# Performance work log

Hardware: AMD Instinct MI355X
Metric: run time of the kernel (lower is better)

The kernel has to match this reference:

```python
import jax, jax.numpy as jnp
import numpy as np
import math

B, L, H, E = 4, 2048, 16, 64

def setup_inputs() -> dict:
    key = jax.random.key(0)
    kq, kk, kv = jax.random.split(key, 3)
    queries = jax.random.normal(kq, (B, L, H, E), dtype=jnp.float32)
    keys = jax.random.normal(kk, (B, L, H, E), dtype=jnp.float32)
    values = jax.random.normal(kv, (B, L, H, E), dtype=jnp.float32)
    return {"queries": queries, "keys": keys, "values": values}

def reference(queries, keys, values):
    # queries: [B,L,H,E], keys: [B,S,H,E], values: [B,S,H,D]
    Bq, Lq, Hq, Eq = queries.shape
    scale = 1.0 / math.sqrt(Eq)
    scores = jnp.einsum('blhe,bshe->bhls', queries, keys)  # [B,H,L,S]
    Sq = keys.shape[1]
    causal = jnp.triu(jnp.ones((Lq, Sq), dtype=bool), k=1)  # True above diagonal
    scores = jnp.where(causal[None, None], -jnp.inf, scores)
    A = jax.nn.softmax(scale * scores, axis=-1)  # dropout is identity in eval
    V = jnp.einsum('bhls,bshd->blhd', A, values)
    return V
```

## Files before the change

### kernel.cpp

```cpp
#include <hip/hip_runtime.h>
#include <hip/hip_bf16.h>

typedef __attribute__((ext_vector_type(8))) short bf16x8;
typedef __attribute__((ext_vector_type(4))) short bf16x4;
typedef __attribute__((ext_vector_type(4))) float f32x4;
typedef __attribute__((ext_vector_type(16))) float f32x16;

#define NB 4
#define NL 2048
#define NH 16
#define NE 64
#define HE (NH*NE)
#define QW 32
#define QBLK 128
#define NQT (NL/QBLK)
#define NPAIR (NQT/2)
#define NBH 64
#define NKT 32
#define TILE_IMG 16384
#define WS_NEED ((size_t)NBH * NKT * TILE_IMG)
#define QSCALE (0.125f * 1.44269504088896340736f)

__device__ __forceinline__ unsigned pk2(float a, float b) {
  float2 t; t.x = a; t.y = b;
  __hip_bfloat162 hh = __float22bfloat162_rn(t);
  union { __hip_bfloat162 h; unsigned u; } v; v.h = hh;
  return v.u;
}
__device__ __forceinline__ void pswap(unsigned &a, unsigned &b) {
  auto r = __builtin_amdgcn_permlane32_swap(a, b, false, false);
  a = r[0]; b = r[1];
}
#define SWZ(row,col) ((row)*128 + ((col) ^ ((((row) ^ ((row)>>2)) & 7) << 4)))

__device__ __forceinline__ void cp16(unsigned char* lds, const unsigned char* g) {
  __builtin_amdgcn_global_load_lds(
      (const __attribute__((address_space(1))) unsigned int*)g,
      (__attribute__((address_space(3))) unsigned int*)lds, 16, 0, 0);
}

__global__ __launch_bounds__(256) void fa_stage(
    const float* __restrict__ K, const float* __restrict__ V,
    unsigned char* __restrict__ img)
{
  const int tid = threadIdx.x;
  const int bid = blockIdx.x;
  const int bh  = bid >> 5;
  const int t0  = bid & 31;
  const int h = bh & (NH-1), b = bh >> 4;
  const size_t base = ((size_t)b * NL * NH + h) * NE + (size_t)(t0 * 64) * HE;
  unsigned char* kimg = img + (size_t)(bh * NKT + t0) * TILE_IMG;
  unsigned char* vimg = kimg + 8192;
  #pragma unroll
  for (int rep = 0; rep < 2; ++rep) {
    const int idx = rep * 256 + tid;
    const int row = idx >> 3, gr = idx & 7;
    const float* kp = K + base + (size_t)row * HE + gr * 8;
    f32x4 a0 = *(const f32x4*)kp;
    f32x4 a1 = *(const f32x4*)(kp + 4);
    union { unsigned u[4]; bf16x8 v; } w;
    w.u[0] = pk2(a0[0], a0[1]); w.u[1] = pk2(a0[2], a0[3]);
    w.u[2] = pk2(a1[0], a1[1]); w.u[3] = pk2(a1[2], a1[3]);
    *(bf16x8*)(kimg + SWZ(row, gr * 16)) = w.v;
  }
  const int trow = tid >> 4, tcol = (tid & 15) * 4, sq = trow * 4;
  f32x4 vr[4];
  #pragma unroll
  for (int i = 0; i < 4; ++i)
    vr[i] = *(const f32x4*)(V + base + (size_t)(sq + i) * HE + tcol);
  #pragma unroll
  for (int j = 0; j < 4; ++j) {
    const int er = tcol + j;
    union { unsigned u[2]; bf16x4 v; } w;
    w.u[0] = pk2(vr[0][j], vr[1][j]);
    w.u[1] = pk2(vr[2][j], vr[3][j]);
    *(bf16x4*)(vimg + SWZ(er, sq * 2)) = w.v;
  }
}

#define PACK(SC, PA0, PA1)                                                     \
      l_run += (((SC[0]+SC[1])+(SC[2]+SC[3]))+((SC[4]+SC[5])+(SC[6]+SC[7])))   \
             + (((SC[8]+SC[9])+(SC[10]+SC[11]))+((SC[12]+SC[13])+(SC[14]+SC[15])));\
      {                                                                        \
        unsigned c0 = pk2(SC[0],SC[1]),   c1 = pk2(SC[2],SC[3]);               \
        unsigned c2 = pk2(SC[4],SC[5]),   c3 = pk2(SC[6],SC[7]);               \
        unsigned c4 = pk2(SC[8],SC[9]),   c5 = pk2(SC[10],SC[11]);             \
        unsigned c6 = pk2(SC[12],SC[13]), c7 = pk2(SC[14],SC[15]);             \
        pswap(c0, c2);  pswap(c1, c3);                                         \
        pswap(c4, c6);  pswap(c5, c7);                                         \
        PA0.u[0]=c0; PA0.u[1]=c1; PA0.u[2]=c2; PA0.u[3]=c3;                    \
        PA1.u[0]=c4; PA1.u[1]=c5; PA1.u[2]=c6; PA1.u[3]=c7;                    \
      }

#define SMPACK(SC, PA0, PA1)                                                   \
      _Pragma("unroll")                                                        \
      for (int r = 0; r < 16; ++r) SC[r] = exp2f(SC[r]);                       \
      PACK(SC, PA0, PA1)

#define STEP(IT, BUF)                                                          \
    {                                                                          \
      if ((IT) + 1 < nt) { asm volatile("s_waitcnt vmcnt(4)" ::: "memory"); }  \
      else               { asm volatile("s_waitcnt vmcnt(0)" ::: "memory"); }  \
      __builtin_amdgcn_sched_barrier(0);                                       \
      __builtin_amdgcn_s_barrier();                                            \
      __builtin_amdgcn_sched_barrier(0);                                       \
      if ((IT) + 2 < nt) {                                                     \
        unsigned char* kd = &k_lds[((BUF)+2)&3][0];                            \
        unsigned char* vd = &v_lds[((BUF)+2)&3][0];                            \
        cp16(kd + wb,        src_pf);                                          \
        cp16(kd + 4096 + wb, src_pf + 4096);                                   \
        cp16(vd + wb,        src_pf + 8192);                                   \
        cp16(vd + 4096 + wb, src_pf + 12288);                                  \
        src_pf += TILE_IMG;                                                    \
      }                                                                        \
      const int kv0 = (IT)*64;                                                 \
      if (kv0 + 63 <= qb) {                                                    \
        f32x16 sc0 = (f32x16)0.0f, sc1 = (f32x16)0.0f;                         \
        _Pragma("unroll")                                                      \
        for (int ks = 0; ks < 4; ++ks) {                                       \
          bf16x8 af0 = *(const bf16x8*)(&k_lds[BUF][0] + addr4[ks]);           \
          bf16x8 af1 = *(const bf16x8*)(&k_lds[BUF][0] + addr4[ks] + 4096);    \
          sc0 = __builtin_amdgcn_mfma_f32_32x32x16_bf16(af0, qf[ks], sc0,0,0,0);\
          sc1 = __builtin_amdgcn_mfma_f32_32x32x16_bf16(af1, qf[ks], sc1,0,0,0);\
        }                                                                      \
        union { unsigned u[4]; bf16x8 v; } a00, a01, a10, a11;                 \
        SMPACK(sc0, a00, a01)                                                  \
        SMPACK(sc1, a10, a11)                                                  \
        _Pragma("unroll")                                                      \
        for (int dt = 0; dt < 2; ++dt) {                                       \
          bf16x8 v00 = *(const bf16x8*)(&v_lds[BUF][0] + addr4[0] + dt*4096);  \
          bf16x8 v01 = *(const bf16x8*)(&v_lds[BUF][0] + addr4[1] + dt*4096);  \
          bf16x8 v10 = *(const bf16x8*)(&v_lds[BUF][0] + addr4[2] + dt*4096);  \
          bf16x8 v11 = *(const bf16x8*)(&v_lds[BUF][0] + addr4[3] + dt*4096);  \
          oacc2[0][dt] = __builtin_amdgcn_mfma_f32_32x32x16_bf16(              \
              v00, a00.v, oacc2[0][dt], 0, 0, 0);                              \
          oacc2[1][dt] = __builtin_amdgcn_mfma_f32_32x32x16_bf16(              \
              v10, a10.v, oacc2[1][dt], 0, 0, 0);                              \
          oacc2[0][dt] = __builtin_amdgcn_mfma_f32_32x32x16_bf16(              \
              v01, a01.v, oacc2[0][dt], 0, 0, 0);                              \
          oacc2[1][dt] = __builtin_amdgcn_mfma_f32_32x32x16_bf16(              \
              v11, a11.v, oacc2[1][dt], 0, 0, 0);                              \
        }                                                                      \
      } else {                                                                 \
        _Pragma("unroll")                                                      \
        for (int sub = 0; sub < 2; ++sub) {                                    \
          const int kv0s = kv0 + sub*32;                                       \
          if (kv0s <= qb + QW - 1) {                                           \
            f32x16 sc = (f32x16)0.0f;                                          \
            _Pragma("unroll")                                                  \
            for (int ks = 0; ks < 4; ++ks) {                                   \
              bf16x8 af = *(const bf16x8*)(&k_lds[BUF][0] + addr4[ks] + sub*4096);\
              sc = __builtin_amdgcn_mfma_f32_32x32x16_bf16(af, qf[ks], sc,0,0,0);\
            }                                                                  \
            _Pragma("unroll")                                                  \
            for (int r = 0; r < 16; ++r) {                                     \
              const int kvg = kv0s + (r&3) + 8*(r>>2) + 4*hi;                  \
              sc[r] = (kvg > qg) ? 0.0f : exp2f(sc[r]);                        \
            }                                                                  \
            union { unsigned u[4]; bf16x8 v; } pa0, pa1;                       \
            PACK(sc, pa0, pa1)                                                 \
            _Pragma("unroll")                                                  \
            for (int dt = 0; dt < 2; ++dt) {                                   \
              _Pragma("unroll")                                                \
              for (int ks2 = 0; ks2 < 2; ++ks2) {                              \
                bf16x8 av = *(const bf16x8*)(&v_lds[BUF][0] +                  \
                    addr4[sub*2 + ks2] + dt*4096);                             \
                oacc2[sub][dt] = __builtin_amdgcn_mfma_f32_32x32x16_bf16(      \
                    av, ks2 ? pa1.v : pa0.v, oacc2[sub][dt], 0, 0, 0);         \
              }                                                                \
            }                                                                  \
          }                                                                    \
        }                                                                      \
      }                                                                        \
    }

#define QTILE_SETUP()                                                          \
    bf16x8 qf[4];                                                              \
    {                                                                          \
      const float* qp = Qb + (size_t)(qb + ln) * HE + hi * 8;                  \
      _Pragma("unroll")                                                        \
      for (int ks = 0; ks < 4; ++ks) {                                         \
        f32x4 a0 = *(const f32x4*)(qp + ks*16);                                \
        f32x4 a1 = *(const f32x4*)(qp + ks*16 + 4);                            \
        union { unsigned u[4]; bf16x8 v; } f;                                  \
        f.u[0] = pk2(a0[0]*QSCALE, a0[1]*QSCALE);                              \
        f.u[1] = pk2(a0[2]*QSCALE, a0[3]*QSCALE);                              \
        f.u[2] = pk2(a1[0]*QSCALE, a1[1]*QSCALE);                              \
        f.u[3] = pk2(a1[2]*QSCALE, a1[3]*QSCALE);                              \
        qf[ks] = f.v;                                                          \
      }                                                                        \
    }                                                                          \
    f32x16 oacc2[2][2];                                                        \
    oacc2[0][0] = (f32x16)0.0f; oacc2[0][1] = (f32x16)0.0f;                    \
    oacc2[1][0] = (f32x16)0.0f; oacc2[1][1] = (f32x16)0.0f;                    \
    float l_run = 0.0f;

__global__ __launch_bounds__(256, 2) void fa_fwd(
    const float* __restrict__ Q, const unsigned char* __restrict__ img,
    float* __restrict__ O)
{
  __shared__ unsigned char k_lds[4][8192];
  __shared__ unsigned char v_lds[4][8192];

  const int tid  = threadIdx.x;
  const int lane = tid & 63;
  const int wid  = tid >> 6;
  const int hi   = lane >> 5;
  const int ln   = lane & 31;

  const int bidp = blockIdx.x;
  const int lb   = (bidp & 7) * 64 + (bidp >> 3);
  const int pair = lb & 7;
  const int bh   = lb >> 3;
  const int h    = bh & (NH-1);
  const int b    = bh >> 4;

  const size_t base = ((size_t)b * NL * NH + h) * NE;
  const float* Qb = Q + base;
  float*       Ob = O + base;
  const unsigned char* bimg = img + (size_t)bh * NKT * TILE_IMG;

  int addr4[4];
  {
    const int F = ((ln ^ (ln >> 2)) & 7) << 4;
    #pragma unroll
    for (int j = 0; j < 4; ++j) addr4[j] = ln*128 + ((j*32 + hi*16) ^ F);
  }
  const int wb = wid << 10;

  #pragma unroll 1
  for (int hf = 0; hf < 2; ++hf) {
    const int qt = hf ? (NQT - 1 - pair) : pair;
    const int q0 = qt * QBLK;
    const int qb = q0 + wid * QW;
    const int nt = qt * 2 + 2;
    const int qg = qb + ln;

    QTILE_SETUP()

    asm volatile("s_waitcnt vmcnt(0)" ::: "memory");
    __builtin_amdgcn_sched_barrier(0);
    __builtin_amdgcn_s_barrier();
    const unsigned char* src_pf = bimg + (size_t)tid * 16;
    cp16(&k_lds[0][0] + wb,        src_pf);
    cp16(&k_lds[0][0] + 4096 + wb, src_pf + 4096);
    cp16(&v_lds[0][0] + wb,        src_pf + 8192);
    cp16(&v_lds[0][0] + 4096 + wb, src_pf + 12288);
    src_pf += TILE_IMG;
    cp16(&k_lds[1][0] + wb,        src_pf);
    cp16(&k_lds[1][0] + 4096 + wb, src_pf + 4096);
    cp16(&v_lds[1][0] + wb,        src_pf + 8192);
    cp16(&v_lds[1][0] + 4096 + wb, src_pf + 12288);
    src_pf += TILE_IMG;

    int bs = 0;
    #pragma unroll 1
    for (; bs + 4 <= nt; bs += 4) {
      STEP(bs + 0, 0)
      STEP(bs + 1, 1)
      STEP(bs + 2, 2)
      STEP(bs + 3, 3)
    }
    if (bs < nt) {
      STEP(bs + 0, 0)
      STEP(bs + 1, 1)
    }

    const float l_tot = l_run + __shfl_xor(l_run, 32);
    const float inv = 1.0f / l_tot;
    float* op = Ob + (size_t)(qb + ln) * HE;
    #pragma unroll
    for (int dt = 0; dt < 2; ++dt)
      #pragma unroll
      for (int rq = 0; rq < 4; ++rq) {
        f32x4 w;
        w[0]=(oacc2[0][dt][rq*4+0]+oacc2[1][dt][rq*4+0])*inv;
        w[1]=(oacc2[0][dt][rq*4+1]+oacc2[1][dt][rq*4+1])*inv;
        w[2]=(oacc2[0][dt][rq*4+2]+oacc2[1][dt][rq*4+2])*inv;
        w[3]=(oacc2[0][dt][rq*4+3]+oacc2[1][dt][rq*4+3])*inv;
        *(f32x4*)(op + dt*32 + 8*rq + 4*hi) = w;
      }
  }
}

__global__ __launch_bounds__(256, 3) void fa_fwd_fused(
    const float* __restrict__ Q, const float* __restrict__ K,
    const float* __restrict__ V, float* __restrict__ O)
{
  __shared__ unsigned char kf_lds[2][64*128];
  __shared__ unsigned char vf_lds[2][64*128];
  const int tid  = threadIdx.x;
  const int lane = tid & 63;
  const int wid  = tid >> 6;
  const int hi   = lane >> 5;
  const int ln   = lane & 31;
  const int trow = tid >> 4;
  const int tcol = (tid & 15) * 4;
  const int sq   = trow * 4;
  const int bidp = blockIdx.x;
  const int lb   = (bidp & 7) * 64 + (bidp >> 3);
  const int pair = lb & 7;
  const int bh   = lb >> 3;
  const int h    = bh & (NH-1);
  const int b    = bh >> 4;
  const size_t base = ((size_t)b * NL * NH + h) * NE;
  const float* Qb = Q + base;
  const float* Kb = K + base;
  const float* Vb = V + base;
  float*       Ob = O + base;
  int cur = 0;
  #pragma unroll 1
  for (int hf = 0; hf < 2; ++hf) {
    const int qt = hf ? (NQT - 1 - pair) : pair;
    const int q0 = qt * QBLK;
    const int qb = q0 + wid * QW;
    const int nt = qt * 2 + 2;
    const int qg = qb + ln;
    bf16x8 qf[4];
    {
      const float* qp = Qb + (size_t)(qb + ln) * HE + hi * 8;
      #pragma unroll
      for (int ks = 0; ks < 4; ++ks) {
        f32x4 a0 = *(const f32x4*)(qp + ks*16);
        f32x4 a1 = *(const f32x4*)(qp + ks*16 + 4);
        union { unsigned u[4]; bf16x8 v; } f;
        f.u[0] = pk2(a0[0]*QSCALE, a0[1]*QSCALE);
        f.u[1] = pk2(a0[2]*QSCALE, a0[3]*QSCALE);
        f.u[2] = pk2(a1[0]*QSCALE, a1[1]*QSCALE);
        f.u[3] = pk2(a1[2]*QSCALE, a1[3]*QSCALE);
        qf[ks] = f.v;
      }
    }
    f32x16 oacc[2];
    oacc[0] = (f32x16)0.0f; oacc[1] = (f32x16)0.0f;
    float l_run = 0.0f;
    f32x4 kreg[4], vreg[4];
    #pragma unroll
    for (int p = 0; p < 4; ++p)
      kreg[p] = *(const f32x4*)(Kb + (size_t)(trow + p*16) * HE + tcol);
    #pragma unroll
    for (int i = 0; i < 4; ++i)
      vreg[i] = *(const f32x4*)(Vb + (size_t)(sq + i) * HE + tcol);
    #pragma unroll 1
    for (int it = 0; it < nt; ++it) {
      unsigned char* kb = kf_lds[cur];
      unsigned char* vb = vf_lds[cur];
      #pragma unroll
      for (int p = 0; p < 4; ++p) {
        const int row = trow + p*16;
        union { unsigned u[2]; bf16x4 v; } w;
        w.u[0] = pk2(kreg[p][0], kreg[p][1]);
        w.u[1] = pk2(kreg[p][2], kreg[p][3]);
        *(bf16x4*)(kb + SWZ(row, tcol*2)) = w.v;
      }
      #pragma unroll
      for (int j = 0; j < 4; ++j) {
        const int er = tcol + j;
        union { unsigned u[2]; bf16x4 v; } w;
        w.u[0] = pk2(vreg[0][j], vreg[1][j]);
        w.u[1] = pk2(vreg[2][j], vreg[3][j]);
        *(bf16x4*)(vb + SWZ(er, sq*2)) = w.v;
      }
      if (it + 1 < nt) {
        const int s0 = (it + 1) * 64;
        #pragma unroll
        for (int p = 0; p < 4; ++p)
          kreg[p] = *(const f32x4*)(Kb + (size_t)(s0 + trow + p*16) * HE + tcol);
        #pragma unroll
        for (int i = 0; i < 4; ++i)
          vreg[i] = *(const f32x4*)(Vb + (size_t)(s0 + sq + i) * HE + tcol);
      }
      asm volatile("s_waitcnt lgkmcnt(0)" ::: "memory");
      __builtin_amdgcn_sched_barrier(0);
      __builtin_amdgcn_s_barrier();
      __builtin_amdgcn_sched_barrier(0);
      #pragma unroll
      for (int sub = 0; sub < 2; ++sub) {
        const int kv0s = it*64 + sub*32;
        if (kv0s <= qb + QW - 1) {
          f32x16 sc = (f32x16)0.0f;
          #pragma unroll
          for (int ks = 0; ks < 4; ++ks) {
            const int kvr = sub*32 + ln;
            bf16x8 af = *(const bf16x8*)(kb + SWZ(kvr, ks*32 + hi*16));
            sc = __builtin_amdgcn_mfma_f32_32x32x16_bf16(af, qf[ks], sc, 0, 0, 0);
          }
          if (kv0s + 31 > qb) {
            #pragma unroll
            for (int r = 0; r < 16; ++r) {
              const int kvg = kv0s + (r&3) + 8*(r>>2) + 4*hi;
              sc[r] = (kvg > qg) ? 0.0f : exp2f(sc[r]);
            }
          } else {
            #pragma unroll
            for (int r = 0; r < 16; ++r) sc[r] = exp2f(sc[r]);
          }
          float s0_ = (sc[0]+sc[1])+(sc[2]+sc[3]);
          float s1_ = (sc[4]+sc[5])+(sc[6]+sc[7]);
          float s2_ = (sc[8]+sc[9])+(sc[10]+sc[11]);
          float s3_ = (sc[12]+sc[13])+(sc[14]+sc[15]);
          l_run += (s0_+s1_)+(s2_+s3_);
          unsigned c0 = pk2(sc[0],sc[1]),   c1 = pk2(sc[2],sc[3]);
          unsigned c2 = pk2(sc[4],sc[5]),   c3 = pk2(sc[6],sc[7]);
          unsigned c4 = pk2(sc[8],sc[9]),   c5 = pk2(sc[10],sc[11]);
          unsigned c6 = pk2(sc[12],sc[13]), c7 = pk2(sc[14],sc[15]);
          pswap(c0, c2);  pswap(c1, c3);
          pswap(c4, c6);  pswap(c5, c7);
          union { unsigned u[4]; bf16x8 v; } pa0, pa1;
          pa0.u[0]=c0; pa0.u[1]=c1; pa0.u[2]=c2; pa0.u[3]=c3;
          pa1.u[0]=c4; pa1.u[1]=c5; pa1.u[2]=c6; pa1.u[3]=c7;
          #pragma unroll
          for (int dt = 0; dt < 2; ++dt) {
            const int dr = dt*32 + ln;
            #pragma unroll
            for (int ks2 = 0; ks2 < 2; ++ks2) {
              bf16x8 av = *(const bf16x8*)(vb + SWZ(dr, sub*64 + ks2*32 + hi*16));
              oacc[dt] = __builtin_amdgcn_mfma_f32_32x32x16_bf16(
                  av, ks2 ? pa1.v : pa0.v, oacc[dt], 0, 0, 0);
            }
          }
        }
      }
      cur ^= 1;
    }
    const float l_tot = l_run + __shfl_xor(l_run, 32);
    const float inv = 1.0f / l_tot;
    float* op = Ob + (size_t)(qb + ln) * HE;
    #pragma unroll
    for (int dt = 0; dt < 2; ++dt)
      #pragma unroll
      for (int rq = 0; rq < 4; ++rq) {
        f32x4 w;
        w[0]=oacc[dt][rq*4+0]*inv; w[1]=oacc[dt][rq*4+1]*inv;
        w[2]=oacc[dt][rq*4+2]*inv; w[3]=oacc[dt][rq*4+3]*inv;
        *(f32x4*)(op + dt*32 + 8*rq + 4*hi) = w;
      }
  }
}

extern "C" void kernel_launch(void* const* d_in, const int* in_sizes, int n_in,
                              void* d_out, int out_size, void* d_ws, size_t ws_size,
                              hipStream_t stream) {
  const float* Q = (const float*)d_in[0];
  const float* K = (const float*)d_in[1];
  const float* V = (const float*)d_in[2];
  float* O = (float*)d_out;
  if (ws_size >= WS_NEED) {
    fa_stage<<<dim3(NBH * NKT), dim3(256), 0, stream>>>(K, V, (unsigned char*)d_ws);
    fa_fwd<<<dim3(NB * NH * NPAIR), dim3(256), 0, stream>>>(
        Q, (const unsigned char*)d_ws, O);
  } else {
    fa_fwd_fused<<<dim3(NB * NH * NPAIR), dim3(256), 0, stream>>>(Q, K, V, O);
  }
}
```

Before: 85.85 us.

## Software-pipeline PV matmul one tile behind QK and compute row sums via MFMA

Restructures the main attention loop so the P·V MFMAs for the previous KV tile run after the current tile's QK^T and exp, keeping the packed probabilities in registers across steps. This lets the exp and pack work overlap with the matrix unit. The scalar row-sum reduction is replaced by MFMAs against an all-ones bf16 fragment, which moves VALU adds onto the matrix core. The denominator is now summed from bf16-rounded probabilities, which slightly changes numerics, and the extra live fragments raise register pressure. The fallback path also changes to a per-step shuffle reduction.

```diff
diff --git a/kernel.cpp b/kernel.cpp
--- a/kernel.cpp
+++ b/kernel.cpp
@@ -20,6 +20,8 @@
 #define TILE_IMG 16384
 #define WS_NEED ((size_t)NBH * NKT * TILE_IMG)
 #define QSCALE (0.125f * 1.44269504088896340736f)
+
+union Pfrag { unsigned u[4]; bf16x8 v; };
 
 __device__ __forceinline__ unsigned pk2(float a, float b) {
   float2 t; t.x = a; t.y = b;
@@ -58,7 +60,7 @@
     const float* kp = K + base + (size_t)row * HE + gr * 8;
     f32x4 a0 = *(const f32x4*)kp;
     f32x4 a1 = *(const f32x4*)(kp + 4);
-    union { unsigned u[4]; bf16x8 v; } w;
+    Pfrag w;
     w.u[0] = pk2(a0[0], a0[1]); w.u[1] = pk2(a0[2], a0[3]);
     w.u[2] = pk2(a1[0], a1[1]); w.u[3] = pk2(a1[2], a1[3]);
     *(bf16x8*)(kimg + SWZ(row, gr * 16)) = w.v;
@@ -79,8 +81,6 @@
 }
 
 #define PACK(SC, PA0, PA1)                                                     \
-      l_run += (((SC[0]+SC[1])+(SC[2]+SC[3]))+((SC[4]+SC[5])+(SC[6]+SC[7])))   \
-             + (((SC[8]+SC[9])+(SC[10]+SC[11]))+((SC[12]+SC[13])+(SC[14]+SC[15])));\
       {                                                                        \
         unsigned c0 = pk2(SC[0],SC[1]),   c1 = pk2(SC[2],SC[3]);               \
         unsigned c2 = pk2(SC[4],SC[5]),   c3 = pk2(SC[6],SC[7]);               \
@@ -90,12 +90,33 @@
         pswap(c4, c6);  pswap(c5, c7);                                         \
         PA0.u[0]=c0; PA0.u[1]=c1; PA0.u[2]=c2; PA0.u[3]=c3;                    \
         PA1.u[0]=c4; PA1.u[1]=c5; PA1.u[2]=c6; PA1.u[3]=c7;                    \
-      }
+      }                                                                        \
+      l_acc = __builtin_amdgcn_mfma_f32_32x32x16_bf16(ones.v, PA0.v, l_acc,0,0,0);\
+      l_acc = __builtin_amdgcn_mfma_f32_32x32x16_bf16(ones.v, PA1.v, l_acc,0,0,0);
 
 #define SMPACK(SC, PA0, PA1)                                                   \
       _Pragma("unroll")                                                        \
       for (int r = 0; r < 16; ++r) SC[r] = exp2f(SC[r]);                       \
       PACK(SC, PA0, PA1)
+
+#define PVSTEP(VBUF)                                                           \
+    {                                                                          \
+      _Pragma("unroll")                                                        \
+      for (int dt = 0; dt < 2; ++dt) {                                         \
+        bf16x8 v00 = *(const bf16x8*)(&v_lds[VBUF][0] + addr4[0] + dt*4096);   \
+        bf16x8 v01 = *(const bf16x8*)(&v_lds[VBUF][0] + addr4[1] + dt*4096);   \
+        bf16x8 v10 = *(const bf16x8*)(&v_lds[VBUF][0] + addr4[2] + dt*4096);   \
+        bf16x8 v11 = *(const bf16x8*)(&v_lds[VBUF][0] + addr4[3] + dt*4096);   \
+        oacc2[0][dt] = __builtin_amdgcn_mfma_f32_32x32x16_bf16(                \
+            v00, p00.v, oacc2[0][dt], 0, 0, 0);                                \
+        oacc2[1][dt] = __builtin_amdgcn_mfma_f32_32x32x16_bf16(                \
+            v10, p10.v, oacc2[1][dt], 0, 0, 0);                                \
+        oacc2[0][dt] = __builtin_amdgcn_mfma_f32_32x32x16_bf16(                \
+            v01, p01.v, oacc2[0][dt], 0, 0, 0);                                \
+        oacc2[1][dt] = __builtin_amdgcn_mfma_f32_32x32x16_bf16(                \
+            v11, p11.v, oacc2[1][dt], 0, 0, 0);                                \
+      }                                                                        \
+    }
 
 #define STEP(IT, BUF)                                                          \
     {                                                                          \
@@ -113,6 +134,7 @@
         cp16(vd + 4096 + wb, src_pf + 12288);                                  \
         src_pf += TILE_IMG;                                                    \
       }                                                                        \
+      Pfrag n00, n01, n10, n11;                                                \
       const int kv0 = (IT)*64;                                                 \
       if (kv0 + 63 <= qb) {                                                    \
         f32x16 sc0 = (f32x16)0.0f, sc1 = (f32x16)0.0f;                         \
@@ -123,55 +145,46 @@
           sc0 = __builtin_amdgcn_mfma_f32_32x32x16_bf16(af0, qf[ks], sc0,0,0,0);\
           sc1 = __builtin_amdgcn_mfma_f32_32x32x16_bf16(af1, qf[ks], sc1,0,0,0);\
         }                                                                      \
-        union { unsigned u[4]; bf16x8 v; } a00, a01, a10, a11;                 \
-        SMPACK(sc0, a00, a01)                                                  \
-        SMPACK(sc1, a10, a11)                                                  \
-        _Pragma("unroll")                                                      \
-        for (int dt = 0; dt < 2; ++dt) {                                       \
-          bf16x8 v00 = *(const bf16x8*)(&v_lds[BUF][0] + addr4[0] + dt*4096);  \
-          bf16x8 v01 = *(const bf16x8*)(&v_lds[BUF][0] + addr4[1] + dt*4096);  \
-          bf16x8 v10 = *(const bf16x8*)(&v_lds[BUF][0] + addr4[2] + dt*4096);  \
-          bf16x8 v11 = *(const bf16x8*)(&v_lds[BUF][0] + addr4[3] + dt*4096);  \
-          oacc2[0][dt] = __builtin_amdgcn_mfma_f32_32x32x16_bf16(              \
-              v00, a00.v, oacc2[0][dt], 0, 0, 0);                              \
-          oacc2[1][dt] = __builtin_amdgcn_mfma_f32_32x32x16_bf16(              \
-              v10, a10.v, oacc2[1][dt], 0, 0, 0);                              \
-          oacc2[0][dt] = __builtin_amdgcn_mfma_f32_32x32x16_bf16(              \
-              v01, a01.v, oacc2[0][dt], 0, 0, 0);                              \
-          oacc2[1][dt] = __builtin_amdgcn_mfma_f32_32x32x16_bf16(              \
-              v11, a11.v, oacc2[1][dt], 0, 0, 0);                              \
+        SMPACK(sc0, n00, n01)                                                  \
+        SMPACK(sc1, n10, n11)                                                  \
+      } else {                                                                 \
+        if (kv0 <= qb + 31) {                                                  \
+          f32x16 sc = (f32x16)0.0f;                                            \
+          _Pragma("unroll")                                                    \
+          for (int ks = 0; ks < 4; ++ks) {                                     \
+            bf16x8 af = *(const bf16x8*)(&k_lds[BUF][0] + addr4[ks]);          \
+            sc = __builtin_amdgcn_mfma_f32_32x32x16_bf16(af, qf[ks], sc,0,0,0);\
+          }                                                                    \
+          _Pragma("unroll")                                                    \
+          for (int r = 0; r < 16; ++r) {                                       \
+            const int kvg = kv0 + (r&3) + 8*(r>>2) + 4*hi;                     \
+            sc[r] = (kvg > qg) ? 0.0f : exp2f(sc[r]);                          \
+          }                                                                    \
+          PACK(sc, n00, n01)                                                   \
+        } else {                                                               \
+          n00.u[0]=0; n00.u[1]=0; n00.u[2]=0; n00.u[3]=0;                      \
+          n01.u[0]=0; n01.u[1]=0; n01.u[2]=0; n01.u[3]=0;                      \
         }                                                                      \
-      } else {                                                                 \
-        _Pragma("unroll")                                                      \
-        for (int sub = 0; sub < 2; ++sub) {                                    \
-          const int kv0s = kv0 + sub*32;                                       \
-          if (kv0s <= qb + QW - 1) {                                           \
-            f32x16 sc = (f32x16)0.0f;                                          \
-            _Pragma("unroll")                                                  \
-            for (int ks = 0; ks < 4; ++ks) {                                   \
-              bf16x8 af = *(const bf16x8*)(&k_lds[BUF][0] + addr4[ks] + sub*4096);\
-              sc = __builtin_amdgcn_mfma_f32_32x32x16_bf16(af, qf[ks], sc,0,0,0);\
-            }                                                                  \
-            _Pragma("unroll")                                                  \
-            for (int r = 0; r < 16; ++r) {                                     \
-              const int kvg = kv0s + (r&3) + 8*(r>>2) + 4*hi;                  \
-              sc[r] = (kvg > qg) ? 0.0f : exp2f(sc[r]);                        \
-            }                                                                  \
-            union { unsigned u[4]; bf16x8 v; } pa0, pa1;                       \
-            PACK(sc, pa0, pa1)                                                 \
-            _Pragma("unroll")                                                  \
-            for (int dt = 0; dt < 2; ++dt) {                                   \
-              _Pragma("unroll")                                                \
-              for (int ks2 = 0; ks2 < 2; ++ks2) {                              \
-                bf16x8 av = *(const bf16x8*)(&v_lds[BUF][0] +                  \
-                    addr4[sub*2 + ks2] + dt*4096);                             \
-                oacc2[sub][dt] = __builtin_amdgcn_mfma_f32_32x32x16_bf16(      \
-                    av, ks2 ? pa1.v : pa0.v, oacc2[sub][dt], 0, 0, 0);         \
-              }                                                                \
-            }                                                                  \
+        if (kv0 + 32 <= qb + 31) {                                             \
+          f32x16 sc = (f32x16)0.0f;                                            \
+          _Pragma("unroll")                                                    \
+          for (int ks = 0; ks < 4; ++ks) {                                     \
+            bf16x8 af = *(const bf16x8*)(&k_lds[BUF][0] + addr4[ks] + 4096);   \
+            sc = __builtin_amdgcn_mfma_f32_32x32x16_bf16(af, qf[ks], sc,0,0,0);\
           }                                                                    \
+          _Pragma("unroll")                                                    \
+          for (int r = 0; r < 16; ++r) {                                       \
+            const int kvg = kv0 + 32 + (r&3) + 8*(r>>2) + 4*hi;                \
+            sc[r] = (kvg > qg) ? 0.0f : exp2f(sc[r]);                          \
+          }                                                                    \
+          PACK(sc, n10, n11)                                                   \
+        } else {                                                               \
+          n10.u[0]=0; n10.u[1]=0; n10.u[2]=0; n10.u[3]=0;                      \
+          n11.u[0]=0; n11.u[1]=0; n11.u[2]=0; n11.u[3]=0;                      \
         }                                                                      \
       }                                                                        \
+      if ((IT) > 0) PVSTEP(((BUF)+3)&3)                                        \
+      p00 = n00; p01 = n01; p10 = n10; p11 = n11;                              \
     }
 
 #define QTILE_SETUP()                                                          \
@@ -182,7 +195,7 @@
       for (int ks = 0; ks < 4; ++ks) {                                         \
         f32x4 a0 = *(const f32x4*)(qp + ks*16);                                \
         f32x4 a1 = *(const f32x4*)(qp + ks*16 + 4);                            \
-        union { unsigned u[4]; bf16x8 v; } f;                                  \
+        Pfrag f;                                                               \
         f.u[0] = pk2(a0[0]*QSCALE, a0[1]*QSCALE);                              \
         f.u[1] = pk2(a0[2]*QSCALE, a0[3]*QSCALE);                              \
         f.u[2] = pk2(a1[0]*QSCALE, a1[1]*QSCALE);                              \
@@ -193,7 +206,10 @@
     f32x16 oacc2[2][2];                                                        \
     oacc2[0][0] = (f32x16)0.0f; oacc2[0][1] = (f32x16)0.0f;                    \
     oacc2[1][0] = (f32x16)0.0f; oacc2[1][1] = (f32x16)0.0f;                    \
-    float l_run = 0.0f;
+    f32x16 l_acc = (f32x16)0.0f;                                               \
+    Pfrag p00, p01, p10, p11;                                                  \
+    p00.u[0]=0;p00.u[1]=0;p00.u[2]=0;p00.u[3]=0;                               \
+    p01=p00; p10=p00; p11=p00;
 
 __global__ __launch_bounds__(256, 2) void fa_fwd(
     const float* __restrict__ Q, const unsigned char* __restrict__ img,
@@ -227,6 +243,10 @@
     for (int j = 0; j < 4; ++j) addr4[j] = ln*128 + ((j*32 + hi*16) ^ F);
   }
   const int wb = wid << 10;
+
+  Pfrag ones;
+  ones.u[0] = 0x3F803F80u; ones.u[1] = 0x3F803F80u;
+  ones.u[2] = 0x3F803F80u; ones.u[3] = 0x3F803F80u;
 
   #pragma unroll 1
   for (int hf = 0; hf < 2; ++hf) {
@@ -265,9 +285,9 @@
       STEP(bs + 0, 0)
       STEP(bs + 1, 1)
     }
-
-    const float l_tot = l_run + __shfl_xor(l_run, 32);
-    const float inv = 1.0f / l_tot;
+    PVSTEP((nt + 3) & 3)
+
+    const float inv = 1.0f / l_acc[0];
     float* op = Ob + (size_t)(qb + ln) * HE;
     #pragma unroll
     for (int dt = 0; dt < 2; ++dt)
@@ -323,7 +343,7 @@
       for (int ks = 0; ks < 4; ++ks) {
         f32x4 a0 = *(const f32x4*)(qp + ks*16);
         f32x4 a1 = *(const f32x4*)(qp + ks*16 + 4);
-        union { unsigned u[4]; bf16x8 v; } f;
+        Pfrag f;
         f.u[0] = pk2(a0[0]*QSCALE, a0[1]*QSCALE);
         f.u[1] = pk2(a0[2]*QSCALE, a0[3]*QSCALE);
         f.u[2] = pk2(a1[0]*QSCALE, a1[1]*QSCALE);
@@ -399,14 +419,16 @@
           float s1_ = (sc[4]+sc[5])+(sc[6]+sc[7]);
           float s2_ = (sc[8]+sc[9])+(sc[10]+sc[11]);
           float s3_ = (sc[12]+sc[13])+(sc[14]+sc[15]);
-          l_run += (s0_+s1_)+(s2_+s3_);
+          float ls = (s0_+s1_)+(s2_+s3_);
+          ls += __shfl_xor(ls, 32);
+          l_run += ls;
           unsigned c0 = pk2(sc[0],sc[1]),   c1 = pk2(sc[2],sc[3]);
           unsigned c2 = pk2(sc[4],sc[5]),   c3 = pk2(sc[6],sc[7]);
           unsigned c4 = pk2(sc[8],sc[9]),   c5 = pk2(sc[10],sc[11]);
           unsigned c6 = pk2(sc[12],sc[13]), c7 = pk2(sc[14],sc[15]);
           pswap(c0, c2);  pswap(c1, c3);
           pswap(c4, c6);  pswap(c5, c7);
-          union { unsigned u[4]; bf16x8 v; } pa0, pa1;
+          Pfrag pa0, pa1;
           pa0.u[0]=c0; pa0.u[1]=c1; pa0.u[2]=c2; pa0.u[3]=c3;
           pa1.u[0]=c4; pa1.u[1]=c5; pa1.u[2]=c6; pa1.u[3]=c7;
           #pragma unroll
@@ -423,8 +445,7 @@
       }
       cur ^= 1;
     }
-    const float l_tot = l_run + __shfl_xor(l_run, 32);
-    const float inv = 1.0f / l_tot;
+    const float inv = 1.0f / l_run;
     float* op = Ob + (size_t)(qb + ln) * HE;
     #pragma unroll
     for (int dt = 0; dt < 2; ++dt)
```

Result: no change. 87.22 us (+1.6%).
